# Optimization experiments

Measured on AMD Instinct MI355X. Metric: run time of the kernel, lower is better.

## Reference

```python
import jax, jax.numpy as jnp
import numpy as np
import math

N_NODES = 50000
N_EDGES = 800000
HIDDEN = 128
NUM_GAUSS = 50
NUM_FILTERS = 128
CUTOFF = 10.0
SHIFT = math.log(2.0)


def setup_inputs() -> dict:
    key = jax.random.key(0)
    ks = jax.random.split(key, 12)
    x = jax.random.normal(ks[0], (N_NODES, HIDDEN), dtype=jnp.float32)
    edge_index = jax.random.randint(ks[1], (2, N_EDGES), 0, N_NODES, dtype=jnp.int64)
    edge_weight = jax.random.uniform(ks[2], (N_EDGES,), dtype=jnp.float32)
    edge_attr = jax.random.normal(ks[3], (N_EDGES, NUM_GAUSS), dtype=jnp.float32)
    # learned parameters (xavier-ish scale)
    def xavier(k, shape):
        fan_in, fan_out = shape[1], shape[0]
        bound = math.sqrt(6.0 / (fan_in + fan_out))
        return jax.random.uniform(k, shape, dtype=jnp.float32, minval=-bound, maxval=bound)
    mlp_w1 = xavier(ks[4], (NUM_FILTERS, NUM_GAUSS))
    mlp_b1 = jnp.zeros((NUM_FILTERS,), jnp.float32)
    mlp_w2 = xavier(ks[5], (NUM_FILTERS, NUM_FILTERS))
    mlp_b2 = jnp.zeros((NUM_FILTERS,), jnp.float32)
    lin1_w = xavier(ks[6], (NUM_FILTERS, HIDDEN))   # no bias
    lin2_w = xavier(ks[7], (HIDDEN, NUM_FILTERS))
    lin2_b = jnp.zeros((HIDDEN,), jnp.float32)
    lin_w = xavier(ks[8], (HIDDEN, HIDDEN))
    lin_b = jnp.zeros((HIDDEN,), jnp.float32)
    return {"x": x, "edge_index": edge_index, "edge_weight": edge_weight,
            "edge_attr": edge_attr, "mlp_w1": mlp_w1, "mlp_b1": mlp_b1,
            "mlp_w2": mlp_w2, "mlp_b2": mlp_b2, "lin1_w": lin1_w,
            "lin2_w": lin2_w, "lin2_b": lin2_b, "lin_w": lin_w, "lin_b": lin_b}


def shifted_softplus(v):
    return jax.nn.softplus(v) - SHIFT


def reference(x, edge_index, edge_weight, edge_attr, mlp_w1, mlp_b1,
              mlp_w2, mlp_b2, lin1_w, lin2_w, lin2_b, lin_w, lin_b):
    src, dst = edge_index[0], edge_index[1]
    # cosine cutoff per edge: [E]
    C = 0.5 * (jnp.cos(edge_weight * (jnp.pi / CUTOFF)) + 1.0)
    # edge filter MLP: [E, num_filters]
    h_e = shifted_softplus(edge_attr @ mlp_w1.T + mlp_b1)
    W = (h_e @ mlp_w2.T + mlp_b2) * C[:, None]
    # node projection, gather-multiply-scatter aggregation
    h = x @ lin1_w.T                       # [N, num_filters]
    msg = h[src] * W                       # [E, num_filters]
    agg = jax.ops.segment_sum(msg, dst, num_segments=N_NODES)  # [N, num_filters]
    h = agg @ lin2_w.T + lin2_b            # [N, hidden]
    h = shifted_softplus(h)
    out = h @ lin_w.T + lin_b              # [N, hidden]
    return out
```

## Files before the change

### kernel.cpp

```cpp
#include <hip/hip_runtime.h>
#include <hip/hip_bf16.h>
#include <math.h>

#define E_NUM 800000
#define NN 50000
#define NG 50
#define NTW (E_NUM / 16)
#define EDGE_BLOCKS 768

typedef __bf16 bf16x8 __attribute__((ext_vector_type(8)));
typedef float f32x4 __attribute__((ext_vector_type(4)));
typedef unsigned short ushortx8 __attribute__((ext_vector_type(8)));

__device__ __forceinline__ unsigned short f2b(float f) {
  union { float f; unsigned u; } v; v.f = f;
  unsigned u = v.u;
  u += 0x7fffu + ((u >> 16) & 1u);
  return (unsigned short)(u >> 16);
}
__device__ __forceinline__ float b2f(unsigned short u) {
  union { unsigned u; float f; } v; v.u = ((unsigned)u) << 16; return v.f;
}
__device__ __forceinline__ float sspf(float v) {
  float e = __builtin_amdgcn_exp2f(-1.4426950408889634f * fabsf(v));
  return fmaxf(v, 0.f) + 0.6931471805599453f * __builtin_amdgcn_logf(fmaf(0.5f, e, 0.5f));
}

__global__ __launch_bounds__(256) void k_hist(const int* __restrict__ ei, int* __restrict__ counts) {
  int e = blockIdx.x * 256 + threadIdx.x;
  if (e < E_NUM) atomicAdd(&counts[ei[E_NUM + e]], 1);
}

__global__ __launch_bounds__(1024) void k_scan(const int* __restrict__ counts,
                                               int* __restrict__ cursor, int* __restrict__ off) {
  __shared__ int tot[1024];
  const int t = threadIdx.x;
  const int C = (NN + 1023) >> 10;
  int lo = t * C, hi = lo + C; if (hi > NN) hi = NN; if (lo > NN) lo = NN;
  int s = 0;
  for (int i = lo; i < hi; ++i) s += counts[i];
  tot[t] = s;
  __syncthreads();
  int mine = s;
  for (int o = 1; o < 1024; o <<= 1) {
    int v = (t >= o) ? tot[t - o] : 0;
    __syncthreads();
    tot[t] += v;
    __syncthreads();
  }
  int run = tot[t] - mine;
  for (int i = lo; i < hi; ++i) { int c = counts[i]; cursor[i] = run; off[i] = run; run += c; }
  if (t == 1023) off[NN] = E_NUM;
}

__global__ __launch_bounds__(256) void k_scatter2(const int* __restrict__ ei, const float* __restrict__ ew,
                                                  int* __restrict__ cursor, int* __restrict__ inv,
                                                  int* __restrict__ srcS, float* __restrict__ cvS) {
  int e = blockIdx.x * 256 + threadIdx.x;
  if (e < E_NUM) {
    int d = ei[E_NUM + e];
    int pos = atomicAdd(&cursor[d], 1);
    inv[e] = pos;
    srcS[pos] = ei[e];
    cvS[pos] = 0.5f * (__builtin_amdgcn_cosf(ew[e] * 0.05f) + 1.f);
  }
}

__global__ __launch_bounds__(256) void k_mfma_gemm(
    const float* __restrict__ X, const float* __restrict__ Wm,
    const float* __restrict__ bias, float* __restrict__ out, int act, int nrows)
{
  __shared__ __attribute__((aligned(16))) unsigned short s_x[128 * 128];
  __shared__ __attribute__((aligned(16))) unsigned short s_w[128 * 128];
  const int tid = threadIdx.x;
  const int w = tid >> 6, lane = tid & 63, q = lane >> 4, n16 = lane & 15;
  const int base = blockIdx.x * 128;

  for (int c = tid; c < 128 * 16; c += 256) {
    int f = c >> 4, ch = c & 15;
    const float4* wp = (const float4*)(Wm + f * 128 + ch * 8);
    float4 v0 = wp[0], v1 = wp[1];
    ushortx8 v = { f2b(v0.x), f2b(v0.y), f2b(v0.z), f2b(v0.w),
                   f2b(v1.x), f2b(v1.y), f2b(v1.z), f2b(v1.w) };
    *(ushortx8*)&s_w[(f << 7) + ((ch ^ (f & 15)) << 3)] = v;
  }
  for (int c = tid; c < 128 * 16; c += 256) {
    int r = c >> 4, ch = c & 15;
    int n = base + r;
    float4 v0 = {0.f, 0.f, 0.f, 0.f}, v1 = v0;
    if (n < nrows) {
      const float4* xp = (const float4*)(X + (long)n * 128 + ch * 8);
      v0 = xp[0]; v1 = xp[1];
    }
    ushortx8 v = { f2b(v0.x), f2b(v0.y), f2b(v0.z), f2b(v0.w),
                   f2b(v1.x), f2b(v1.y), f2b(v1.z), f2b(v1.w) };
    *(ushortx8*)&s_x[(r << 7) + ((ch ^ (r & 15)) << 3)] = v;
  }
  __syncthreads();

  float bv[8];
#pragma unroll
  for (int t = 0; t < 8; ++t) bv[t] = bias ? bias[t * 16 + n16] : 0.f;

  bf16x8 a[2][4];
#pragma unroll
  for (int g = 0; g < 2; ++g) {
    int r = w * 32 + g * 16 + n16;
#pragma unroll
    for (int ks = 0; ks < 4; ++ks)
      a[g][ks] = *(const bf16x8*)&s_x[(r << 7) + (((ks * 4 + q) ^ (r & 15)) << 3)];
  }
#pragma unroll
  for (int t = 0; t < 8; ++t) {
    int f = t * 16 + n16;
    bf16x8 b[4];
#pragma unroll
    for (int ks = 0; ks < 4; ++ks)
      b[ks] = *(const bf16x8*)&s_w[(f << 7) + (((ks * 4 + q) ^ (f & 15)) << 3)];
#pragma unroll
    for (int g = 0; g < 2; ++g) {
      f32x4 acc = {0.f, 0.f, 0.f, 0.f};
#pragma unroll
      for (int ks = 0; ks < 4; ++ks)
        acc = __builtin_amdgcn_mfma_f32_16x16x32_bf16(a[g][ks], b[ks], acc, 0, 0, 0);
#pragma unroll
      for (int r = 0; r < 4; ++r) {
        int n = base + w * 32 + g * 16 + q * 4 + r;
        if (n < nrows) {
          float v = acc[r] + bv[t];
          if (act) v = sspf(v);
          out[(long)n * 128 + f] = v;
        }
      }
    }
  }
}

__global__ __launch_bounds__(256, 3) void k_edge2(
    const float* __restrict__ attr, const int* __restrict__ ei,
    const float* __restrict__ ew, const float* __restrict__ w1,
    const float* __restrict__ b1, const float* __restrict__ w2,
    const float* __restrict__ b2, const float* __restrict__ h,
    const int* __restrict__ inv, float* __restrict__ agg,
    unsigned short* __restrict__ Wsrt, int mode)
{
  __shared__ __attribute__((aligned(16))) unsigned short s_w2[128 * 128];
  __shared__ __attribute__((aligned(16))) unsigned short s_scr[4 * 16 * 136];

  const int tid  = threadIdx.x;
  const int w    = tid >> 6;
  const int lane = tid & 63;
  const int q    = lane >> 4;
  const int n16  = lane & 15;

  for (int i = tid; i < 128 * 128; i += 256) {
    int f = i >> 7, k = i & 127;
    int pos = (f << 7) + ((((k >> 3) ^ (f & 15)) << 3)) + (k & 7);
    s_w2[pos] = f2b(w2[i]);
  }
  bf16x8 w1A[8], w1B[8];
#pragma unroll
  for (int t = 0; t < 8; ++t) {
    int f = t * 16 + n16;
    const float* row = w1 + f * NG;
    union { ushortx8 u; bf16x8 b; } ua, ub;
#pragma unroll
    for (int j = 0; j < 8; ++j) ua.u[j] = f2b(row[q * 8 + j]);
#pragma unroll
    for (int j = 0; j < 8; ++j) { int k = 32 + q * 8 + j; ub.u[j] = (k < NG) ? f2b(row[k]) : (unsigned short)0; }
    w1A[t] = ua.b; w1B[t] = ub.b;
  }
  float b1v[8], b2v[8];
#pragma unroll
  for (int t = 0; t < 8; ++t) {
    b1v[t] = b1[t * 16 + n16];
    b2v[t] = b2[t * 16 + n16];
  }
  __syncthreads();

  unsigned short* scr = s_scr + w * (16 * 136);
  const int nwaves = EDGE_BLOCKS * 4;
  const int gw = blockIdx.x * 4 + w;

  for (int tile = gw; tile < NTW; tile += nwaves) {
    const int e0 = tile * 16;
    const int er = e0 + n16;
    const float* rp = attr + (long)er * NG;

    float2 p0 = *(const float2*)(rp + q * 8);
    float2 p1 = *(const float2*)(rp + q * 8 + 2);
    float2 p2 = *(const float2*)(rp + q * 8 + 4);
    float2 p3 = *(const float2*)(rp + q * 8 + 6);
    float2 p4 = {0.f, 0.f}, p5 = {0.f, 0.f}, p6 = {0.f, 0.f}, p7 = {0.f, 0.f};
    if (q < 2) {
      const float* rp2 = rp + 32 + q * 8;
      p4 = *(const float2*)(rp2);
      p5 = *(const float2*)(rp2 + 2);
      p6 = *(const float2*)(rp2 + 4);
      p7 = *(const float2*)(rp2 + 6);
    } else if (q == 2) {
      p4 = *(const float2*)(rp + 48);
    }
    union { ushortx8 u; bf16x8 b; } ua, ub;
    ua.u[0] = f2b(p0.x); ua.u[1] = f2b(p0.y); ua.u[2] = f2b(p1.x); ua.u[3] = f2b(p1.y);
    ua.u[4] = f2b(p2.x); ua.u[5] = f2b(p2.y); ua.u[6] = f2b(p3.x); ua.u[7] = f2b(p3.y);
    ub.u[0] = f2b(p4.x); ub.u[1] = f2b(p4.y); ub.u[2] = f2b(p5.x); ub.u[3] = f2b(p5.y);
    ub.u[4] = f2b(p6.x); ub.u[5] = f2b(p6.y); ub.u[6] = f2b(p7.x); ub.u[7] = f2b(p7.y);

#pragma unroll
    for (int t = 0; t < 8; ++t) {
      f32x4 acc = {0.f, 0.f, 0.f, 0.f};
      acc = __builtin_amdgcn_mfma_f32_16x16x32_bf16(ua.b, w1A[t], acc, 0, 0, 0);
      acc = __builtin_amdgcn_mfma_f32_16x16x32_bf16(ub.b, w1B[t], acc, 0, 0, 0);
      int f = t * 16 + n16;
#pragma unroll
      for (int r = 0; r < 4; ++r) {
        int row = q * 4 + r;
        scr[row * 136 + f] = f2b(sspf(acc[r] + b1v[t]));
      }
    }
    __builtin_amdgcn_wave_barrier();

    bf16x8 a2f[4];
#pragma unroll
    for (int ks = 0; ks < 4; ++ks)
      a2f[ks] = *(const bf16x8*)&scr[n16 * 136 + ks * 32 + q * 8];
    __builtin_amdgcn_wave_barrier();

    int srcv[4], dstv[4]; float cvv[4];
    if (mode == 0) {
#pragma unroll
      for (int r = 0; r < 4; ++r) {
        int e = e0 + q * 4 + r;
        srcv[r] = ei[e];
        dstv[r] = ei[E_NUM + e];
        cvv[r] = 0.5f * (__builtin_amdgcn_cosf(ew[e] * 0.05f) + 1.f);
      }
    }

#pragma unroll
    for (int t = 0; t < 8; ++t) {
      int f = t * 16 + n16;
      f32x4 acc = {0.f, 0.f, 0.f, 0.f};
#pragma unroll
      for (int ks = 0; ks < 4; ++ks) {
        bf16x8 bb = *(const bf16x8*)&s_w2[(f << 7) + (((ks * 4 + q) ^ (f & 15)) << 3)];
        acc = __builtin_amdgcn_mfma_f32_16x16x32_bf16(a2f[ks], bb, acc, 0, 0, 0);
      }
      if (mode == 1) {
#pragma unroll
        for (int r = 0; r < 4; ++r) {
          int row = q * 4 + r;
          scr[row * 136 + f] = f2b(acc[r] + b2v[t]);
        }
      } else {
#pragma unroll
        for (int r = 0; r < 4; ++r) {
          float msg = h[(long)srcv[r] * 128 + f] * (acc[r] + b2v[t]) * cvv[r];
          atomicAdd(&agg[(long)dstv[r] * 128 + f], msg);
        }
      }
    }

    if (mode == 1) {
      __builtin_amdgcn_wave_barrier();
#pragma unroll
      for (int i = 0; i < 4; ++i) {
        int row = i * 4 + q;
        int pos = inv[e0 + row];
        ushortx8 v = *(const ushortx8*)&scr[row * 136 + n16 * 8];
        *(ushortx8*)(Wsrt + (long)pos * 128 + n16 * 8) = v;
      }
      __builtin_amdgcn_wave_barrier();
    }
  }
}

__global__ __launch_bounds__(256) void k_e2(
    const unsigned short* __restrict__ Wsrt, const int* __restrict__ srcS,
    const float* __restrict__ cvS, const int* __restrict__ off,
    const float* __restrict__ h, float* __restrict__ agg)
{
  const int wv = threadIdx.x >> 6, lane = threadIdx.x & 63;
  const int n = blockIdx.x * 4 + wv;
  const int j0 = off[n], j1 = off[n + 1];
  float ax = 0.f, ay = 0.f;
  for (int j = j0; j < j1; ++j) {
    int s = srcS[j];
    float c = cvS[j];
    unsigned wp = *(const unsigned*)(Wsrt + (long)j * 128 + lane * 2);
    float2 hp = *(const float2*)(h + (long)s * 128 + lane * 2);
    ax += c * hp.x * b2f((unsigned short)(wp & 0xffffu));
    ay += c * hp.y * b2f((unsigned short)(wp >> 16));
  }
  float2 o; o.x = ax; o.y = ay;
  *(float2*)(agg + (long)n * 128 + lane * 2) = o;
}

extern "C" void kernel_launch(void* const* d_in, const int* in_sizes, int n_in,
                              void* d_out, int out_size, void* d_ws, size_t ws_size,
                              hipStream_t stream) {
  const float* x     = (const float*)d_in[0];
  const int*   ei    = (const int*)  d_in[1];
  const float* ew    = (const float*)d_in[2];
  const float* attr  = (const float*)d_in[3];
  const float* w1    = (const float*)d_in[4];
  const float* b1    = (const float*)d_in[5];
  const float* w2    = (const float*)d_in[6];
  const float* b2    = (const float*)d_in[7];
  const float* lin1w = (const float*)d_in[8];
  const float* lin2w = (const float*)d_in[9];
  const float* lin2b = (const float*)d_in[10];
  const float* linw  = (const float*)d_in[11];
  const float* linb  = (const float*)d_in[12];
  float* out = (float*)d_out;

  char* base = (char*)d_ws;
  float* agg    = (float*)base;
  float* h      = agg + (size_t)NN * 128;
  int*   counts = (int*)(h + (size_t)NN * 128);
  int*   cursor = counts + NN;
  int*   off    = cursor + NN;
  int*   inv    = off + NN + 1;
  int*   srcS   = inv + E_NUM;
  float* cvS    = (float*)(srcS + E_NUM);
  size_t head   = (size_t)((char*)(cvS + E_NUM) - base);
  size_t woff   = (head + 255) & ~(size_t)255;
  unsigned short* Wsrt = (unsigned short*)(base + woff);
  size_t need = woff + (size_t)E_NUM * 128 * sizeof(unsigned short);
  const int mode = (ws_size >= need) ? 1 : 0;

  const int gemm_grid = (NN + 127) / 128;
  if (mode == 1) {
    (void)hipMemsetAsync(counts, 0, (size_t)NN * sizeof(int), stream);
    k_hist<<<(E_NUM + 255) / 256, 256, 0, stream>>>(ei, counts);
    k_scan<<<1, 1024, 0, stream>>>(counts, cursor, off);
    k_scatter2<<<(E_NUM + 255) / 256, 256, 0, stream>>>(ei, ew, cursor, inv, srcS, cvS);
    k_edge2<<<EDGE_BLOCKS, 256, 0, stream>>>(attr, ei, ew, w1, b1, w2, b2, h, inv, agg, Wsrt, 1);
    k_mfma_gemm<<<gemm_grid, 256, 0, stream>>>(x, lin1w, nullptr, h, 0, NN);
    k_e2<<<NN / 4, 256, 0, stream>>>(Wsrt, srcS, cvS, off, h, agg);
  } else {
    (void)hipMemsetAsync(agg, 0, (size_t)NN * 128 * sizeof(float), stream);
    k_mfma_gemm<<<gemm_grid, 256, 0, stream>>>(x, lin1w, nullptr, h, 0, NN);
    k_edge2<<<EDGE_BLOCKS, 256, 0, stream>>>(attr, ei, ew, w1, b1, w2, b2, h, inv, agg, Wsrt, 0);
  }
  k_mfma_gemm<<<gemm_grid, 256, 0, stream>>>(agg, lin2w, lin2b, h, 1, NN);
  k_mfma_gemm<<<gemm_grid, 256, 0, stream>>>(h, linw, linb, out, 0, NN);
}
```

Before: 713.6 us.

## Fold cosine cutoff into edge filter and unroll CSR aggregation with nontemporal loads

The cosine cutoff is now multiplied into the edge filter values before they are stored as bf16 in the destination-sorted buffer, so the separate per-edge cvS array and its scatter write go away. The aggregation kernel no longer loads cvS and processes four edges per iteration, issuing independent loads to expose memory-level parallelism. The filter buffer is written and read with nontemporal hints so it does not pollute cache. Rounding the product to bf16 instead of multiplying in fp32 changes numerics slightly.

```diff
diff --git a/kernel.cpp b/kernel.cpp
--- a/kernel.cpp
+++ b/kernel.cpp
@@ -53,16 +53,15 @@
   if (t == 1023) off[NN] = E_NUM;
 }
 
-__global__ __launch_bounds__(256) void k_scatter2(const int* __restrict__ ei, const float* __restrict__ ew,
+__global__ __launch_bounds__(256) void k_scatter2(const int* __restrict__ ei,
                                                   int* __restrict__ cursor, int* __restrict__ inv,
-                                                  int* __restrict__ srcS, float* __restrict__ cvS) {
+                                                  int* __restrict__ srcS) {
   int e = blockIdx.x * 256 + threadIdx.x;
   if (e < E_NUM) {
     int d = ei[E_NUM + e];
     int pos = atomicAdd(&cursor[d], 1);
     inv[e] = pos;
     srcS[pos] = ei[e];
-    cvS[pos] = 0.5f * (__builtin_amdgcn_cosf(ew[e] * 0.05f) + 1.f);
   }
 }
 
@@ -227,14 +226,17 @@
       a2f[ks] = *(const bf16x8*)&scr[n16 * 136 + ks * 32 + q * 8];
     __builtin_amdgcn_wave_barrier();
 
-    int srcv[4], dstv[4]; float cvv[4];
+    float cvv[4];
+#pragma unroll
+    for (int r = 0; r < 4; ++r)
+      cvv[r] = 0.5f * (__builtin_amdgcn_cosf(ew[e0 + q * 4 + r] * 0.05f) + 1.f);
+
+    int srcv[4], dstv[4];
     if (mode == 0) {
 #pragma unroll
       for (int r = 0; r < 4; ++r) {
-        int e = e0 + q * 4 + r;
-        srcv[r] = ei[e];
-        dstv[r] = ei[E_NUM + e];
-        cvv[r] = 0.5f * (__builtin_amdgcn_cosf(ew[e] * 0.05f) + 1.f);
+        srcv[r] = ei[e0 + q * 4 + r];
+        dstv[r] = ei[E_NUM + e0 + q * 4 + r];
       }
     }
 
@@ -251,7 +253,7 @@
 #pragma unroll
         for (int r = 0; r < 4; ++r) {
           int row = q * 4 + r;
-          scr[row * 136 + f] = f2b(acc[r] + b2v[t]);
+          scr[row * 136 + f] = f2b((acc[r] + b2v[t]) * cvv[r]);
         }
       } else {
 #pragma unroll
@@ -269,7 +271,7 @@
         int row = i * 4 + q;
         int pos = inv[e0 + row];
         ushortx8 v = *(const ushortx8*)&scr[row * 136 + n16 * 8];
-        *(ushortx8*)(Wsrt + (long)pos * 128 + n16 * 8) = v;
+        __builtin_nontemporal_store(v, (ushortx8*)(Wsrt + (long)pos * 128 + n16 * 8));
       }
       __builtin_amdgcn_wave_barrier();
     }
@@ -278,20 +280,34 @@
 
 __global__ __launch_bounds__(256) void k_e2(
     const unsigned short* __restrict__ Wsrt, const int* __restrict__ srcS,
-    const float* __restrict__ cvS, const int* __restrict__ off,
-    const float* __restrict__ h, float* __restrict__ agg)
+    const int* __restrict__ off, const float* __restrict__ h, float* __restrict__ agg)
 {
   const int wv = threadIdx.x >> 6, lane = threadIdx.x & 63;
   const int n = blockIdx.x * 4 + wv;
   const int j0 = off[n], j1 = off[n + 1];
   float ax = 0.f, ay = 0.f;
-  for (int j = j0; j < j1; ++j) {
+  int j = j0;
+  for (; j + 4 <= j1; j += 4) {
+    int s0 = srcS[j], s1 = srcS[j + 1], s2 = srcS[j + 2], s3 = srcS[j + 3];
+    unsigned w0 = __builtin_nontemporal_load((const unsigned*)(Wsrt + (long)(j    ) * 128) + lane);
+    unsigned w1_ = __builtin_nontemporal_load((const unsigned*)(Wsrt + (long)(j + 1) * 128) + lane);
+    unsigned w2_ = __builtin_nontemporal_load((const unsigned*)(Wsrt + (long)(j + 2) * 128) + lane);
+    unsigned w3_ = __builtin_nontemporal_load((const unsigned*)(Wsrt + (long)(j + 3) * 128) + lane);
+    float2 h0 = *(const float2*)(h + (long)s0 * 128 + lane * 2);
+    float2 h1 = *(const float2*)(h + (long)s1 * 128 + lane * 2);
+    float2 h2 = *(const float2*)(h + (long)s2 * 128 + lane * 2);
+    float2 h3 = *(const float2*)(h + (long)s3 * 128 + lane * 2);
+    ax += h0.x * b2f((unsigned short)(w0 & 0xffffu)) + h1.x * b2f((unsigned short)(w1_ & 0xffffu))
+        + h2.x * b2f((unsigned short)(w2_ & 0xffffu)) + h3.x * b2f((unsigned short)(w3_ & 0xffffu));
+    ay += h0.y * b2f((unsigned short)(w0 >> 16)) + h1.y * b2f((unsigned short)(w1_ >> 16))
+        + h2.y * b2f((unsigned short)(w2_ >> 16)) + h3.y * b2f((unsigned short)(w3_ >> 16));
+  }
+  for (; j < j1; ++j) {
     int s = srcS[j];
-    float c = cvS[j];
-    unsigned wp = *(const unsigned*)(Wsrt + (long)j * 128 + lane * 2);
+    unsigned wp = __builtin_nontemporal_load((const unsigned*)(Wsrt + (long)j * 128) + lane);
     float2 hp = *(const float2*)(h + (long)s * 128 + lane * 2);
-    ax += c * hp.x * b2f((unsigned short)(wp & 0xffffu));
-    ay += c * hp.y * b2f((unsigned short)(wp >> 16));
+    ax += hp.x * b2f((unsigned short)(wp & 0xffffu));
+    ay += hp.y * b2f((unsigned short)(wp >> 16));
   }
   float2 o; o.x = ax; o.y = ay;
   *(float2*)(agg + (long)n * 128 + lane * 2) = o;
@@ -323,8 +339,7 @@
   int*   off    = cursor + NN;
   int*   inv    = off + NN + 1;
   int*   srcS   = inv + E_NUM;
-  float* cvS    = (float*)(srcS + E_NUM);
-  size_t head   = (size_t)((char*)(cvS + E_NUM) - base);
+  size_t head   = (size_t)((char*)(srcS + E_NUM) - base);
   size_t woff   = (head + 255) & ~(size_t)255;
   unsigned short* Wsrt = (unsigned short*)(base + woff);
   size_t need = woff + (size_t)E_NUM * 128 * sizeof(unsigned short);
@@ -335,10 +350,10 @@
     (void)hipMemsetAsync(counts, 0, (size_t)NN * sizeof(int), stream);
     k_hist<<<(E_NUM + 255) / 256, 256, 0, stream>>>(ei, counts);
     k_scan<<<1, 1024, 0, stream>>>(counts, cursor, off);
-    k_scatter2<<<(E_NUM + 255) / 256, 256, 0, stream>>>(ei, ew, cursor, inv, srcS, cvS);
+    k_scatter2<<<(E_NUM + 255) / 256, 256, 0, stream>>>(ei, cursor, inv, srcS);
     k_edge2<<<EDGE_BLOCKS, 256, 0, stream>>>(attr, ei, ew, w1, b1, w2, b2, h, inv, agg, Wsrt, 1);
     k_mfma_gemm<<<gemm_grid, 256, 0, stream>>>(x, lin1w, nullptr, h, 0, NN);
-    k_e2<<<NN / 4, 256, 0, stream>>>(Wsrt, srcS, cvS, off, h, agg);
+    k_e2<<<NN / 4, 256, 0, stream>>>(Wsrt, srcS, off, h, agg);
   } else {
     (void)hipMemsetAsync(agg, 0, (size_t)NN * 128 * sizeof(float), stream);
     k_mfma_gemm<<<gemm_grid, 256, 0, stream>>>(x, lin1w, nullptr, h, 0, NN);
```

Result: faster. 668.8 us (-6.3%).
